# Performance work log

Hardware: AMD Instinct MI355X
Metric: run time of the kernel (lower is better)

The kernel has to match this reference:

```python
import jax, jax.numpy as jnp
import numpy as np

V, C, H, L, BLK = 32000, 1024, 16, 4, 1024
B, T = 4, 1024
FF = 100
HD = C // H
EPS = 1e-5


def setup_inputs() -> dict:
    key = jax.random.key(0)
    ks = jax.random.split(key, 16)
    n = lambda k, s: (jax.random.normal(k, s, dtype=jnp.float32) * 0.02)
    inp = {
        "idx": jax.random.randint(ks[0], (B, T), 0, V),
        "tok_emb": n(ks[1], (V, C)),
        "pos_emb": n(ks[2], (BLK, C)),
        "Wq": n(ks[3], (L, C, C)), "bq": jnp.zeros((L, C)),
        "Wk": n(ks[4], (L, C, C)), "bk": jnp.zeros((L, C)),
        "Wv": n(ks[5], (L, C, C)), "bv": jnp.zeros((L, C)),
        "Wo": n(ks[6], (L, C, C)), "bo": jnp.zeros((L, C)),
        "ln1_w": jnp.ones((L, C)), "ln1_b": jnp.zeros((L, C)),
        "ln2_w": jnp.ones((L, C)), "ln2_b": jnp.zeros((L, C)),
        "W1": n(ks[7], (L, C, FF)), "b1": jnp.zeros((L, FF)),
        "W2": n(ks[8], (L, FF, C)), "b2": jnp.zeros((L, C)),
        "lnf_w": jnp.ones((C,)), "lnf_b": jnp.zeros((C,)),
    }
    return inp


def _ln(x, w, b):
    m = jnp.mean(x, -1, keepdims=True)
    v = jnp.mean(jnp.square(x - m), -1, keepdims=True)
    return (x - m) * jax.lax.rsqrt(v + EPS) * w + b


def reference(idx, tok_emb, pos_emb, Wq, bq, Wk, bk, Wv, bv, Wo, bo,
              ln1_w, ln1_b, ln2_w, ln2_b, W1, b1, W2, b2, lnf_w, lnf_b):
    Bn, Tn = idx.shape
    x = tok_emb[idx] + pos_emb[:Tn][None]  # [B,T,C]; dropout is identity at eval
    scale = 1.0 / np.sqrt(HD).astype(np.float32)
    att_maps = []
    for l in range(L):
        h = _ln(x, ln1_w[l], ln1_b[l])
        q = (h @ Wq[l] + bq[l]).reshape(Bn, Tn, H, HD).transpose(0, 2, 1, 3)
        k = (h @ Wk[l] + bk[l]).reshape(Bn, Tn, H, HD).transpose(0, 2, 1, 3)
        v = (h @ Wv[l] + bv[l]).reshape(Bn, Tn, H, HD).transpose(0, 2, 1, 3)
        att = jax.nn.softmax(jnp.einsum("bhqd,bhkd->bhqk", q, k) * scale, axis=-1)
        y = jnp.einsum("bhqk,bhkd->bhqd", att, v).transpose(0, 2, 1, 3).reshape(Bn, Tn, C)
        x = x + (y @ Wo[l] + bo[l])
        f = _ln(x, ln2_w[l], ln2_b[l])
        f = jax.nn.relu(f @ W1[l] + b1[l]) @ W2[l] + b2[l]
        x = x + f
        att_maps.append(att.mean(0))  # [H,T,T]
    x = _ln(x, lnf_w, lnf_b)
    pooled = x.mean(1)  # [B,C]
    return pooled, jnp.stack(att_maps)  # [L,H,T,T]
```

## Files before the change

### kernel.cpp

```cpp
#include <hip/hip_runtime.h>

typedef __bf16 bf16;
typedef __bf16 bf16x4 __attribute__((ext_vector_type(4)));
typedef __bf16 bf16x8 __attribute__((ext_vector_type(8)));
typedef float  f32x4  __attribute__((ext_vector_type(4)));

static constexpr int kC   = 1024;
static constexpr int kT   = 1024;
static constexpr int kB   = 4;
static constexpr int kH   = 16;
static constexpr int kHD  = 64;
static constexpr int kL   = 4;
static constexpr int kFF  = 100;
static constexpr int kFFP = 128;
static constexpr int kM   = kB * kT;

__device__ __forceinline__ void gload16(const bf16* g, bf16* l)
{
    __builtin_amdgcn_global_load_lds(
        (const __attribute__((address_space(1))) void*)g,
        (__attribute__((address_space(3))) void*)l, 16, 0, 0);
}

__device__ __forceinline__ unsigned bpack(float a, float b)
{
    bf16 x = (bf16)a, y = (bf16)b;
    unsigned short ux = __builtin_bit_cast(unsigned short, x);
    unsigned short uy = __builtin_bit_cast(unsigned short, y);
    return (unsigned)ux | ((unsigned)uy << 16);
}
__device__ __forceinline__ float blo(unsigned u) { return __builtin_bit_cast(float, u << 16); }
__device__ __forceinline__ float bhi(unsigned u) { return __builtin_bit_cast(float, u & 0xffff0000u); }

__global__ __launch_bounds__(256)
void prep_kernel(const float* __restrict__ Wq, const float* __restrict__ Wk,
                 const float* __restrict__ Wv, const float* __restrict__ Wo,
                 const float* __restrict__ W1, const float* __restrict__ W2,
                 const float* __restrict__ bq, const float* __restrict__ bk,
                 const float* __restrict__ bv,
                 bf16* __restrict__ WQKVT, bf16* __restrict__ WOT,
                 bf16* __restrict__ W1T, bf16* __restrict__ W2T,
                 float* __restrict__ BQKV, float* __restrict__ pooled)
{
    __shared__ float tile[32][33];
    const int bid = blockIdx.x, tid = threadIdx.x;
    const float* src; bf16* dst; int K, N, KP, NP, bx, by;
    if (bid < 12288) {
        const int slab = bid >> 10, within = bid & 1023;
        const int l = slab / 3, which = slab % 3;
        const float* W = (which == 0) ? Wq : (which == 1) ? Wk : Wv;
        src = W + (long)l * kC * kC;
        dst = WQKVT + (long)l * 3 * kC * kC + (long)which * kC * kC;
        K = N = KP = NP = kC; bx = within & 31; by = within >> 5;
    } else if (bid < 16384) {
        const int t = bid - 12288, z = t >> 10, within = t & 1023;
        src = Wo + (long)z * kC * kC; dst = WOT + (long)z * kC * kC;
        K = N = KP = NP = kC; bx = within & 31; by = within >> 5;
    } else if (bid < 16896) {
        const int t = bid - 16384, z = t >> 7, within = t & 127;
        src = W1 + (long)z * kC * kFF; dst = W1T + (long)z * kFFP * kC;
        K = kC; N = kFF; KP = kC; NP = kFFP; bx = within & 3; by = within >> 2;
    } else if (bid < 17408) {
        const int t = bid - 16896, z = t >> 7, within = t & 127;
        src = W2 + (long)z * kFF * kC; dst = W2T + (long)z * kC * kFFP;
        K = kFF; N = kC; KP = kFFP; NP = kC; bx = within & 31; by = within >> 5;
    } else if (bid < 17456) {
        const int gid = (bid - 17408) * 256 + tid;
        const int l = gid / (3 * kC), wq = (gid / kC) % 3, c = gid & (kC - 1);
        const float* s = (wq == 0) ? bq : (wq == 1) ? bk : bv;
        BQKV[gid] = s[l * kC + c];
        return;
    } else {
        const int i = (bid - 17456) * 256 + tid;
        if (i < kB * kC) pooled[i] = 0.f;
        return;
    }
    const int n0 = bx * 32, k0 = by * 32;
    const int tx = tid & 31, ty = tid >> 5;
#pragma unroll
    for (int i = 0; i < 4; ++i) {
        int k = k0 + ty + i * 8, n = n0 + tx;
        tile[ty + i * 8][tx] = (k < K && n < N) ? src[(long)k * N + n] : 0.f;
    }
    __syncthreads();
#pragma unroll
    for (int i = 0; i < 4; ++i) {
        int n = n0 + ty + i * 8, k = k0 + tx;
        if (n < NP && k < KP) dst[(long)n * KP + k] = (bf16)tile[tx][ty + i * 8];
    }
}

__global__ __launch_bounds__(256)
void embed_kernel(const int* __restrict__ idx, const float* __restrict__ tok,
                  const float* __restrict__ pos, float* __restrict__ x)
{
    const int m = blockIdx.x;
    const int c = threadIdx.x * 4;
    const int t = m & (kT - 1);
    const long tk = (long)idx[m] * kC;
    float4 a = *(const float4*)&tok[tk + c];
    float4 b = *(const float4*)&pos[(long)t * kC + c];
    float4 o; o.x = a.x + b.x; o.y = a.y + b.y; o.z = a.z + b.z; o.w = a.w + b.w;
    *(float4*)&x[(long)m * kC + c] = o;
}

__global__ __launch_bounds__(256)
void ln_kernel(const float* __restrict__ x, const float* __restrict__ g,
               const float* __restrict__ be, bf16* __restrict__ ob)
{
    __shared__ float red[8];
    const long row = blockIdx.x;
    const int tid = threadIdx.x, lane = tid & 63, wv = tid >> 6;
    const float4 v = *(const float4*)&x[row * kC + tid * 4];
    float s = v.x + v.y + v.z + v.w;
    float s2 = v.x * v.x + v.y * v.y + v.z * v.z + v.w * v.w;
#pragma unroll
    for (int o = 32; o > 0; o >>= 1) { s += __shfl_down(s, o); s2 += __shfl_down(s2, o); }
    if (!lane) { red[wv] = s; red[4 + wv] = s2; }
    __syncthreads();
    s  = red[0] + red[1] + red[2] + red[3];
    s2 = red[4] + red[5] + red[6] + red[7];
    const float mean = s * (1.f / kC);
    const float var  = s2 * (1.f / kC) - mean * mean;
    const float rstd = rsqrtf(var + 1e-5f);
    const float4 gg = *(const float4*)&g[tid * 4];
    const float4 bb = *(const float4*)&be[tid * 4];
    bf16x4 o;
    o[0] = (bf16)((v.x - mean) * rstd * gg.x + bb.x);
    o[1] = (bf16)((v.y - mean) * rstd * gg.y + bb.y);
    o[2] = (bf16)((v.z - mean) * rstd * gg.z + bb.z);
    o[3] = (bf16)((v.w - mean) * rstd * gg.w + bb.w);
    *(bf16x4*)&ob[row * kC + tid * 4] = o;
}

template<int WAVES_M, int WAVES_N, int AI, int BJ, int MODE, int GL>
__global__ __launch_bounds__(256)
void gemm_bf16(const bf16* __restrict__ Ag, long strideA,
               const bf16* __restrict__ Bg, long strideB,
               const float* __restrict__ bias, int strideBias,
               bf16* __restrict__ outb, long strideOut,
               float* __restrict__ resid,
               int N, int K, int lda, int ldb)
{
    constexpr int BM = WAVES_M * AI * 16;
    constexpr int BN = WAVES_N * BJ * 16;
    constexpr int BK = 64;
    constexpr int LK = GL ? BK : (BK + 8);
    __shared__ __align__(16) bf16 As[BM * LK];
    __shared__ __align__(16) bf16 Bs[BN * LK];
    const int tid = threadIdx.x, lane = tid & 63, wv = tid >> 6;
    const int wm = wv / WAVES_N, wn = wv % WAVES_N;
    const int lr = lane & 15, lg = lane >> 4;
    const int z = blockIdx.z;
    const bf16* A = Ag + (long)z * strideA;
    const bf16* B = Bg + (long)z * strideB;
    const float* bi = bias ? bias + (long)z * strideBias : nullptr;
    const int m0 = blockIdx.y * BM, n0 = blockIdx.x * BN;

    f32x4 acc[AI][BJ];
#pragma unroll
    for (int i = 0; i < AI; ++i)
#pragma unroll
        for (int j = 0; j < BJ; ++j) acc[i][j] = (f32x4){0.f, 0.f, 0.f, 0.f};

    for (int k0 = 0; k0 < K; k0 += BK) {
        if constexpr (GL) {
            static_assert((BM % 32) == 0 && (BN % 32) == 0, "GL tile multiple of 32");
            const int sr  = lane >> 3;
            const int gcb = (lane & 7) ^ sr;
            constexpr int ARW = BM / 4;
            constexpr int BRW = BN / 4;
#pragma unroll
            for (int p = 0; p < BM / 32; ++p)
                gload16(A + (long)(m0 + wv * ARW + p * 8 + sr) * lda + k0 + gcb * 8,
                        &As[(wv * ARW + p * 8) * BK]);
#pragma unroll
            for (int p = 0; p < BN / 32; ++p)
                gload16(B + (long)(n0 + wv * BRW + p * 8 + sr) * ldb + k0 + gcb * 8,
                        &Bs[(wv * BRW + p * 8) * BK]);
        } else {
            constexpr int AP = (BM * BK) / (256 * 8);
#pragma unroll
            for (int p = 0; p < AP; ++p) {
                int r = p * 32 + (tid >> 3), c = (tid & 7) * 8;
                *(uint4*)&As[r * LK + c] = *(const uint4*)&A[(long)(m0 + r) * lda + k0 + c];
            }
            constexpr int BP = (BN * BK) / (256 * 8);
#pragma unroll
            for (int p = 0; p < BP; ++p) {
                int r = p * 32 + (tid >> 3), c = (tid & 7) * 8;
                *(uint4*)&Bs[r * LK + c] = *(const uint4*)&B[(long)(n0 + r) * ldb + k0 + c];
            }
        }
        __syncthreads();
#pragma unroll
        for (int kk = 0; kk < 2; ++kk) {
            bf16x8 af[AI], bfv[BJ];
#pragma unroll
            for (int i = 0; i < AI; ++i) {
                const int r = wm * AI * 16 + i * 16 + lr;
                const int c = GL ? (((kk * 4 + lg) ^ (lr & 7)) * 8) : (kk * 32 + lg * 8);
                af[i] = *(const bf16x8*)&As[r * LK + c];
            }
#pragma unroll
            for (int j = 0; j < BJ; ++j) {
                const int r = wn * BJ * 16 + j * 16 + lr;
                const int c = GL ? (((kk * 4 + lg) ^ (lr & 7)) * 8) : (kk * 32 + lg * 8);
                bfv[j] = *(const bf16x8*)&Bs[r * LK + c];
            }
#pragma unroll
            for (int i = 0; i < AI; ++i)
#pragma unroll
                for (int j = 0; j < BJ; ++j)
                    acc[i][j] = __builtin_amdgcn_mfma_f32_16x16x32_bf16(af[i], bfv[j], acc[i][j], 0, 0, 0);
        }
        __syncthreads();
    }

#pragma unroll
    for (int i = 0; i < AI; ++i)
#pragma unroll
        for (int j = 0; j < BJ; ++j)
#pragma unroll
            for (int rr = 0; rr < 4; ++rr) {
                const int grow = m0 + wm * AI * 16 + i * 16 + lg * 4 + rr;
                const int gcol = n0 + wn * BJ * 16 + j * 16 + lr;
                float v = acc[i][j][rr];
                if constexpr (MODE == 0) {
                    v += bi[gcol];
                    if (z == 0) v *= 0.125f * 1.44269504f;
                    const int b = grow >> 10, t = grow & (kT - 1);
                    const int hh = gcol >> 6, hd = gcol & 63;
                    long o = (long)z * strideOut;
                    if (z == 2) o += (((long)b * kH + hh) * kHD + hd) * kT + t;
                    else        o += (((long)b * kH + hh) * kT + t) * kHD + hd;
                    outb[o] = (bf16)v;
                } else {
                    v += bi[gcol];
                    resid[(long)grow * N + gcol] += v;
                }
            }
}

__global__ __launch_bounds__(256, 2)
void ff_fused(float* __restrict__ X, const float* __restrict__ g,
              const float* __restrict__ be,
              const bf16* __restrict__ W1T_, const float* __restrict__ b1_,
              const bf16* __restrict__ W2T_, const float* __restrict__ b2_)
{
    __shared__ __align__(16) bf16 Hs[16 * kC];
    __shared__ __align__(16) bf16 F1s[16 * kFFP];
    const int tid = threadIdx.x, lane = tid & 63, w = tid >> 6;
    const int lr = lane & 15, lg = lane >> 4;
    const int r0 = blockIdx.x * 16;

    {
        const int row = tid >> 4, c16 = tid & 15;
        float4 xv[16];
        float s1 = 0.f, s2 = 0.f;
#pragma unroll
        for (int p = 0; p < 8; ++p) {
            const float* base = &X[(long)(r0 + row) * kC + p * 128 + c16 * 8];
            xv[2 * p]     = *(const float4*)base;
            xv[2 * p + 1] = *(const float4*)(base + 4);
#pragma unroll
            for (int e = 0; e < 4; ++e) {
                float a0 = ((const float*)&xv[2 * p])[e], a1 = ((const float*)&xv[2 * p + 1])[e];
                s1 += a0 + a1; s2 += a0 * a0 + a1 * a1;
            }
        }
#pragma unroll
        for (int off = 1; off < 16; off <<= 1) { s1 += __shfl_xor(s1, off); s2 += __shfl_xor(s2, off); }
        const float mean = s1 * (1.f / kC);
        const float rstd = rsqrtf(s2 * (1.f / kC) - mean * mean + 1e-5f);
#pragma unroll
        for (int p = 0; p < 8; ++p) {
            const int c0 = p * 128 + c16 * 8;
            float4 g0 = *(const float4*)&g[c0],  g1 = *(const float4*)&g[c0 + 4];
            float4 b0 = *(const float4*)&be[c0], b1v = *(const float4*)&be[c0 + 4];
            float h[8];
#pragma unroll
            for (int e = 0; e < 4; ++e) {
                h[e]     = (((const float*)&xv[2 * p])[e]     - mean) * rstd * ((const float*)&g0)[e] + ((const float*)&b0)[e];
                h[4 + e] = (((const float*)&xv[2 * p + 1])[e] - mean) * rstd * ((const float*)&g1)[e] + ((const float*)&b1v)[e];
            }
            uint4 hv;
            hv.x = bpack(h[0], h[1]); hv.y = bpack(h[2], h[3]);
            hv.z = bpack(h[4], h[5]); hv.w = bpack(h[6], h[7]);
            const int cb = c16 + p * 16;
            *(uint4*)&Hs[row * kC + ((cb ^ (row & 7)) << 3)] = hv;
        }
    }
    __syncthreads();

    {
        f32x4 accA[2], accB[2];
#pragma unroll
        for (int j = 0; j < 2; ++j) { accA[j] = (f32x4){0,0,0,0}; accB[j] = (f32x4){0,0,0,0}; }
        for (int k0 = 0; k0 < kC; k0 += 64) {
            const bf16x8 a0 = *(const bf16x8*)&Hs[lr * kC + ((((k0 >> 3) + 0 * 4 + lg) ^ (lr & 7)) << 3)];
            const bf16x8 a1 = *(const bf16x8*)&Hs[lr * kC + ((((k0 >> 3) + 1 * 4 + lg) ^ (lr & 7)) << 3)];
#pragma unroll
            for (int j = 0; j < 2; ++j) {
                const bf16x8 b0 = *(const bf16x8*)&W1T_[(long)(w * 32 + j * 16 + lr) * kC + k0 + 0 * 32 + lg * 8];
                const bf16x8 b1 = *(const bf16x8*)&W1T_[(long)(w * 32 + j * 16 + lr) * kC + k0 + 1 * 32 + lg * 8];
                accA[j] = __builtin_amdgcn_mfma_f32_16x16x32_bf16(a0, b0, accA[j], 0, 0, 0);
                accB[j] = __builtin_amdgcn_mfma_f32_16x16x32_bf16(a1, b1, accB[j], 0, 0, 0);
            }
        }
#pragma unroll
        for (int j = 0; j < 2; ++j)
#pragma unroll
            for (int rr = 0; rr < 4; ++rr) {
                const int row = lg * 4 + rr, col = w * 32 + j * 16 + lr;
                float v = accA[j][rr] + accB[j][rr] + (col < kFF ? b1_[col] : 0.f);
                F1s[row * kFFP + (((col >> 3) ^ (row & 7)) << 3) + (col & 7)] = (bf16)fmaxf(v, 0.f);
            }
    }
    __syncthreads();

    for (int nc = 0; nc < 8; ++nc) {
        f32x4 acc[2];
        acc[0] = (f32x4){0.f, 0.f, 0.f, 0.f};
        acc[1] = (f32x4){0.f, 0.f, 0.f, 0.f};
#pragma unroll
        for (int kk = 0; kk < 4; ++kk) {
            const bf16x8 a = *(const bf16x8*)&F1s[lr * kFFP + (((kk * 4 + lg) ^ (lr & 7)) << 3)];
#pragma unroll
            for (int j = 0; j < 2; ++j) {
                const bf16x8 bv = *(const bf16x8*)&W2T_[(long)(nc * 128 + w * 32 + j * 16 + lr) * kFFP + kk * 32 + lg * 8];
                acc[j] = __builtin_amdgcn_mfma_f32_16x16x32_bf16(a, bv, acc[j], 0, 0, 0);
            }
        }
#pragma unroll
        for (int j = 0; j < 2; ++j)
#pragma unroll
            for (int rr = 0; rr < 4; ++rr) {
                const int row = r0 + lg * 4 + rr, col = nc * 128 + w * 32 + j * 16 + lr;
                X[(long)row * kC + col] += acc[j][rr] + b2_[col];
            }
    }
}

__global__ __launch_bounds__(256, 2)
void attn_fused(const bf16* __restrict__ Qg, const bf16* __restrict__ Kg,
                const bf16* __restrict__ VTg, bf16* __restrict__ yg,
                float* __restrict__ attm)
{
    __shared__ __align__(16) bf16 SH[32768];
    bf16* Klds = SH;
    bf16* Vlds = SH + 8192;
    bf16* Ps   = SH + 16384;
    __shared__ __align__(16) float reds[16][4];
    __shared__ float invs[16];
    const int tid = threadIdx.x, lane = tid & 63, w = tid >> 6;
    const int lr = lane & 15, lg = lane >> 4;
    const int bid = blockIdx.x, r_ = bid >> 3;
    const int h = ((bid & 7) << 1) | (r_ & 1);
    const int q0 = (r_ >> 1) * 16;

    const int sr  = lane >> 3;
    const int gcb = (lane & 7) ^ sr;
    const int loB = (lg & 1) * 4;

    unsigned am_[16][2];
#pragma unroll
    for (int j = 0; j < 16; ++j) { am_[j][0] = 0u; am_[j][1] = 0u; }

    for (int b = 0; b < kB; ++b) {
        const long bh = (long)b * kH + h;
        const bf16* Qb = Qg + (bh * kT + q0) * kHD;
        const bf16* Kb = Kg + bh * kT * kHD;
        const bf16* Vb = VTg + bh * (long)kHD * kT;

        const bf16x8 qf0 = *(const bf16x8*)&Qb[lr * kHD + lg * 8];
        const bf16x8 qf1 = *(const bf16x8*)&Qb[lr * kHD + 32 + lg * 8];

        {
            const int rowb = w * 16 + sr;
            gload16(Kb + (rowb)     * kHD + gcb * 8, &Klds[(w * 16) * 64]);
            gload16(Kb + (rowb + 8) * kHD + gcb * 8, &Klds[(w * 16 + 8) * 64]);
            gload16(Vb + (long)(rowb)     * kT + gcb * 8, &Vlds[(w * 16) * 64]);
            gload16(Vb + (long)(rowb + 8) * kT + gcb * 8, &Vlds[(w * 16 + 8) * 64]);
        }
        __syncthreads();

        float s = 0.f;
        f32x4 y0 = (f32x4){0.f, 0.f, 0.f, 0.f};
        f32x4 y1 = (f32x4){0.f, 0.f, 0.f, 0.f};

        for (int kt = 0; kt < 16; ++kt) {
            const int cur = (kt & 1) * 4096;
            if (kt < 15) {
                const int nxt = 4096 - cur;
                const int kn = (kt + 1) * 64;
                const int rowb = w * 16 + sr;
                gload16(Kb + (kn + rowb)     * kHD + gcb * 8, &Klds[nxt + (w * 16) * 64]);
                gload16(Kb + (kn + rowb + 8) * kHD + gcb * 8, &Klds[nxt + (w * 16 + 8) * 64]);
                gload16(Vb + (long)(rowb)     * kT + kn + gcb * 8, &Vlds[nxt + (w * 16) * 64]);
                gload16(Vb + (long)(rowb + 8) * kT + kn + gcb * 8, &Vlds[nxt + (w * 16 + 8) * 64]);
            }
            const int krow = w * 16 + lr;
            const bf16x8 kf0 = *(const bf16x8*)&Klds[cur + krow * 64 + (((0 + lg) ^ (lr & 7)) << 3)];
            const bf16x8 kf1 = *(const bf16x8*)&Klds[cur + krow * 64 + (((4 + lg) ^ (lr & 7)) << 3)];
            f32x4 a = (f32x4){0.f, 0.f, 0.f, 0.f};
            a = __builtin_amdgcn_mfma_f32_16x16x32_bf16(kf0, qf0, a, 0, 0, 0);
            a = __builtin_amdgcn_mfma_f32_16x16x32_bf16(kf1, qf1, a, 0, 0, 0);
            const float e0 = exp2f(a[0]), e1 = exp2f(a[1]);
            const float e2 = exp2f(a[2]), e3 = exp2f(a[3]);
            s += (e0 + e1) + (e2 + e3);
            const int tb = kt * 8 + w * 2 + (lg >> 1);
            uint2 pk; pk.x = bpack(e0, e1); pk.y = bpack(e2, e3);
            *(uint2*)&Ps[lr * kT + ((tb ^ (lr & 7)) << 3) + loB] = pk;
            __syncthreads();
            const int vrow = w * 16 + lr;
            const bf16x8 a0 = *(const bf16x8*)&Ps[lr * kT + (((kt * 8 + 0 + lg) ^ (lr & 7)) << 3)];
            const bf16x8 v0 = *(const bf16x8*)&Vlds[cur + vrow * 64 + (((0 + lg) ^ (lr & 7)) << 3)];
            const bf16x8 a1 = *(const bf16x8*)&Ps[lr * kT + (((kt * 8 + 4 + lg) ^ (lr & 7)) << 3)];
            const bf16x8 v1 = *(const bf16x8*)&Vlds[cur + vrow * 64 + (((4 + lg) ^ (lr & 7)) << 3)];
            y0 = __builtin_amdgcn_mfma_f32_16x16x32_bf16(a0, v0, y0, 0, 0, 0);
            y1 = __builtin_amdgcn_mfma_f32_16x16x32_bf16(a1, v1, y1, 0, 0, 0);
            __syncthreads();
        }

        s += __shfl_xor(s, 16);
        s += __shfl_xor(s, 32);
        if (lane < 16) reds[lane][w] = s;
        __syncthreads();
        float4 rv = *(const float4*)&reds[lr][0];
        const float inv = __builtin_amdgcn_rcpf((rv.x + rv.y) + (rv.z + rv.w));
        const float iv4 = inv * 0.25f;
        if (lane < 16) invs[lane] = inv;

#pragma unroll
        for (int kt = 0; kt < 16; ++kt) {
            const int tb = kt * 8 + w * 2 + (lg >> 1);
            uint2 e2v = *(const uint2*)&Ps[lr * kT + ((tb ^ (lr & 7)) << 3) + loB];
#pragma unroll
            for (int d = 0; d < 2; ++d) {
                unsigned ev = d ? e2v.y : e2v.x;
                unsigned av = am_[kt][d];
                float n0 = blo(av) + blo(ev) * iv4;
                float n1 = bhi(av) + bhi(ev) * iv4;
                am_[kt][d] = bpack(n0, n1);
            }
        }

#pragma unroll
        for (int rr = 0; rr < 4; ++rr) {
            const float iv = invs[lg * 4 + rr];
            yg[((long)b * kT + q0 + lg * 4 + rr) * kC + h * kHD + w * 16 + lr]
                = (bf16)((y0[rr] + y1[rr]) * iv);
        }
    }

    __syncthreads();
    float* amf = (float*)SH;
#pragma unroll
    for (int kt = 0; kt < 16; ++kt)
#pragma unroll
        for (int d = 0; d < 2; ++d) {
            unsigned av = am_[kt][d];
            const int col = kt * 64 + w * 16 + lg * 4 + 2 * d;
            amf[lr * kT + col]     = blo(av);
            amf[lr * kT + col + 1] = bhi(av);
        }
    __syncthreads();
#pragma unroll
    for (int p = 0; p < 16; ++p) {
        const int f = p * 256 + tid;
        const int row = f >> 8, c4 = f & 255;
        float4 v = *(const float4*)&amf[row * kT + c4 * 4];
        *(float4*)&attm[((long)h * kT + q0 + row) * kT + c4 * 4] = v;
    }
}

__global__ __launch_bounds__(256)
void pool_kernel(const bf16* __restrict__ hb, float* __restrict__ pooled)
{
    const int c = blockIdx.x * 256 + threadIdx.x;
    const int b = blockIdx.y;
    const int t0 = blockIdx.z * 128;
    float s = 0.f;
    for (int t = t0; t < t0 + 128; ++t) s += (float)hb[((long)b * kT + t) * kC + c];
    atomicAdd(&pooled[b * kC + c], s * (1.f / kT));
}

extern "C" void kernel_launch(void* const* d_in, const int* in_sizes, int n_in,
                              void* d_out, int out_size, void* d_ws, size_t ws_size,
                              hipStream_t stream)
{
    const int*   idx  = (const int*)d_in[0];
    const float* tok  = (const float*)d_in[1];
    const float* pos  = (const float*)d_in[2];
    const float* Wq   = (const float*)d_in[3];
    const float* bq   = (const float*)d_in[4];
    const float* Wk   = (const float*)d_in[5];
    const float* bk   = (const float*)d_in[6];
    const float* Wv   = (const float*)d_in[7];
    const float* bv   = (const float*)d_in[8];
    const float* Wo   = (const float*)d_in[9];
    const float* bo   = (const float*)d_in[10];
    const float* ln1w = (const float*)d_in[11];
    const float* ln1b = (const float*)d_in[12];
    const float* ln2w = (const float*)d_in[13];
    const float* ln2b = (const float*)d_in[14];
    const float* W1   = (const float*)d_in[15];
    const float* b1   = (const float*)d_in[16];
    const float* W2   = (const float*)d_in[17];
    const float* b2   = (const float*)d_in[18];
    const float* lnfw = (const float*)d_in[19];
    const float* lnfb = (const float*)d_in[20];

    char* ws = (char*)d_ws;
    long off = 0;
    auto alloc = [&](long bytes) { char* p = ws + off; off += (bytes + 255) & ~255L; return p; };
    bf16*  WQKVT = (bf16*)alloc((long)kL * 3 * kC * kC * 2);
    bf16*  WOT   = (bf16*)alloc((long)kL * kC * kC * 2);
    bf16*  W1T   = (bf16*)alloc((long)kL * kFFP * kC * 2);
    bf16*  W2T   = (bf16*)alloc((long)kL * kC * kFFP * 2);
    float* BQKV  = (float*)alloc((long)kL * 3 * kC * 4);
    float* X     = (float*)alloc((long)kM * kC * 4);
    bf16*  Hbuf  = (bf16*)alloc((long)kM * kC * 2);
    bf16*  QKV   = (bf16*)alloc(3L * kM * kC * 2);
    bf16*  Y     = (bf16*)alloc((long)kM * kC * 2);

    float* pooled = (float*)d_out;
    float* attm_base = pooled + kB * kC;

    prep_kernel<<<17472, 256, 0, stream>>>(Wq, Wk, Wv, Wo, W1, W2, bq, bk, bv,
                                           WQKVT, WOT, W1T, W2T, BQKV, pooled);
    embed_kernel<<<kM, 256, 0, stream>>>(idx, tok, pos, X);

    for (int l = 0; l < kL; ++l) {
        ln_kernel<<<kM, 256, 0, stream>>>(X, ln1w + l * kC, ln1b + l * kC, Hbuf);
        gemm_bf16<2, 2, 4, 4, 0, 1><<<dim3(8, 32, 3), 256, 0, stream>>>(
            Hbuf, 0L, WQKVT + (long)l * 3 * kC * kC, (long)kC * kC,
            BQKV + l * 3 * kC, kC, QKV, (long)kM * kC, nullptr,
            kC, kC, kC, kC);
        attn_fused<<<dim3(1024), 256, 0, stream>>>(
            QKV, QKV + (long)kM * kC, QKV + 2L * kM * kC, Y,
            attm_base + (long)l * kH * kT * kT);
        gemm_bf16<2, 2, 4, 4, 4, 1><<<dim3(8, 32, 1), 256, 0, stream>>>(
            Y, 0L, WOT + (long)l * kC * kC, 0L, bo + l * kC, 0,
            nullptr, 0L, X, kC, kC, kC, kC);
        ff_fused<<<256, 256, 0, stream>>>(X, ln2w + l * kC, ln2b + l * kC,
                                          W1T + (long)l * kFFP * kC, b1 + l * kFF,
                                          W2T + (long)l * kC * kFFP, b2 + l * kC);
    }
    ln_kernel<<<kM, 256, 0, stream>>>(X, lnfw, lnfb, Hbuf);
    pool_kernel<<<dim3(4, kB, 8), 256, 0, stream>>>(Hbuf, pooled);
}
```

Before: 916.1 us.

## Prefetch next batch K/V tile and drop per-iteration trailing barrier in attention

The attention kernel now issues the first K/V tile load for the next batch during the last key tile of the current batch, so the double buffer runs continuously across the batch loop instead of stalling at each batch start. The trailing __syncthreads in each key-tile iteration is removed. This relies on each wave reading only the K/V rows it loaded itself, guarded by explicit s_waitcnt vmcnt counts. The mid-iteration barrier becomes an lgkmcnt wait plus a raw s_barrier with sched_barrier fences, and the key loop is fully unrolled. The risks are fragile hand-counted vmcnt waits and higher register pressure from the unroll.

```diff
diff --git a/kernel.cpp b/kernel.cpp
--- a/kernel.cpp
+++ b/kernel.cpp
@@ -362,44 +362,60 @@
     const int sr  = lane >> 3;
     const int gcb = (lane & 7) ^ sr;
     const int loB = (lg & 1) * 4;
+    const int rowb = w * 16 + sr;
+    const int ldK0 = (w * 16) * 64, ldK1 = (w * 16 + 8) * 64;
 
     unsigned am_[16][2];
 #pragma unroll
     for (int j = 0; j < 16; ++j) { am_[j][0] = 0u; am_[j][1] = 0u; }
+
+    {
+        const bf16* Kb0 = Kg + (long)h * kT * kHD;
+        const bf16* Vb0 = VTg + (long)h * kHD * kT;
+        gload16(Kb0 + (rowb)     * kHD + gcb * 8, &Klds[ldK0]);
+        gload16(Kb0 + (rowb + 8) * kHD + gcb * 8, &Klds[ldK1]);
+        gload16(Vb0 + (long)(rowb)     * kT + gcb * 8, &Vlds[ldK0]);
+        gload16(Vb0 + (long)(rowb + 8) * kT + gcb * 8, &Vlds[ldK1]);
+    }
 
     for (int b = 0; b < kB; ++b) {
         const long bh = (long)b * kH + h;
         const bf16* Qb = Qg + (bh * kT + q0) * kHD;
         const bf16* Kb = Kg + bh * kT * kHD;
         const bf16* Vb = VTg + bh * (long)kHD * kT;
+        const bf16* Kbn = Kg + (bh + kH) * kT * kHD;
+        const bf16* Vbn = VTg + (bh + kH) * (long)kHD * kT;
 
         const bf16x8 qf0 = *(const bf16x8*)&Qb[lr * kHD + lg * 8];
         const bf16x8 qf1 = *(const bf16x8*)&Qb[lr * kHD + 32 + lg * 8];
-
-        {
-            const int rowb = w * 16 + sr;
-            gload16(Kb + (rowb)     * kHD + gcb * 8, &Klds[(w * 16) * 64]);
-            gload16(Kb + (rowb + 8) * kHD + gcb * 8, &Klds[(w * 16 + 8) * 64]);
-            gload16(Vb + (long)(rowb)     * kT + gcb * 8, &Vlds[(w * 16) * 64]);
-            gload16(Vb + (long)(rowb + 8) * kT + gcb * 8, &Vlds[(w * 16 + 8) * 64]);
-        }
-        __syncthreads();
 
         float s = 0.f;
         f32x4 y0 = (f32x4){0.f, 0.f, 0.f, 0.f};
         f32x4 y1 = (f32x4){0.f, 0.f, 0.f, 0.f};
 
+#pragma unroll
         for (int kt = 0; kt < 16; ++kt) {
-            const int cur = (kt & 1) * 4096;
+            const int cur = ((b * 16 + kt) & 1) * 4096;
+            const int nxt = 4096 - cur;
             if (kt < 15) {
-                const int nxt = 4096 - cur;
                 const int kn = (kt + 1) * 64;
-                const int rowb = w * 16 + sr;
-                gload16(Kb + (kn + rowb)     * kHD + gcb * 8, &Klds[nxt + (w * 16) * 64]);
-                gload16(Kb + (kn + rowb + 8) * kHD + gcb * 8, &Klds[nxt + (w * 16 + 8) * 64]);
-                gload16(Vb + (long)(rowb)     * kT + kn + gcb * 8, &Vlds[nxt + (w * 16) * 64]);
-                gload16(Vb + (long)(rowb + 8) * kT + kn + gcb * 8, &Vlds[nxt + (w * 16 + 8) * 64]);
-            }
+                gload16(Kb + (kn + rowb)     * kHD + gcb * 8, &Klds[nxt + ldK0]);
+                gload16(Kb + (kn + rowb + 8) * kHD + gcb * 8, &Klds[nxt + ldK1]);
+                gload16(Vb + (long)(rowb)     * kT + kn + gcb * 8, &Vlds[nxt + ldK0]);
+                gload16(Vb + (long)(rowb + 8) * kT + kn + gcb * 8, &Vlds[nxt + ldK1]);
+            } else if (b < kB - 1) {
+                gload16(Kbn + (rowb)     * kHD + gcb * 8, &Klds[nxt + ldK0]);
+                gload16(Kbn + (rowb + 8) * kHD + gcb * 8, &Klds[nxt + ldK1]);
+                gload16(Vbn + (long)(rowb)     * kT + gcb * 8, &Vlds[nxt + ldK0]);
+                gload16(Vbn + (long)(rowb + 8) * kT + gcb * 8, &Vlds[nxt + ldK1]);
+            }
+            if (kt == 15 && b == kB - 1) {
+                asm volatile("s_waitcnt vmcnt(0)" ::: "memory");
+            } else {
+                asm volatile("s_waitcnt vmcnt(4)" ::: "memory");
+            }
+            __builtin_amdgcn_sched_barrier(0);
+
             const int krow = w * 16 + lr;
             const bf16x8 kf0 = *(const bf16x8*)&Klds[cur + krow * 64 + (((0 + lg) ^ (lr & 7)) << 3)];
             const bf16x8 kf1 = *(const bf16x8*)&Klds[cur + krow * 64 + (((4 + lg) ^ (lr & 7)) << 3)];
@@ -412,7 +428,11 @@
             const int tb = kt * 8 + w * 2 + (lg >> 1);
             uint2 pk; pk.x = bpack(e0, e1); pk.y = bpack(e2, e3);
             *(uint2*)&Ps[lr * kT + ((tb ^ (lr & 7)) << 3) + loB] = pk;
-            __syncthreads();
+
+            asm volatile("s_waitcnt lgkmcnt(0)" ::: "memory");
+            __builtin_amdgcn_s_barrier();
+            __builtin_amdgcn_sched_barrier(0);
+
             const int vrow = w * 16 + lr;
             const bf16x8 a0 = *(const bf16x8*)&Ps[lr * kT + (((kt * 8 + 0 + lg) ^ (lr & 7)) << 3)];
             const bf16x8 v0 = *(const bf16x8*)&Vlds[cur + vrow * 64 + (((0 + lg) ^ (lr & 7)) << 3)];
@@ -420,13 +440,14 @@
             const bf16x8 v1 = *(const bf16x8*)&Vlds[cur + vrow * 64 + (((4 + lg) ^ (lr & 7)) << 3)];
             y0 = __builtin_amdgcn_mfma_f32_16x16x32_bf16(a0, v0, y0, 0, 0, 0);
             y1 = __builtin_amdgcn_mfma_f32_16x16x32_bf16(a1, v1, y1, 0, 0, 0);
-            __syncthreads();
         }
 
         s += __shfl_xor(s, 16);
         s += __shfl_xor(s, 32);
         if (lane < 16) reds[lane][w] = s;
-        __syncthreads();
+        asm volatile("s_waitcnt lgkmcnt(0)" ::: "memory");
+        __builtin_amdgcn_s_barrier();
+        __builtin_amdgcn_sched_barrier(0);
         float4 rv = *(const float4*)&reds[lr][0];
         const float inv = __builtin_amdgcn_rcpf((rv.x + rv.y) + (rv.z + rv.w));
         const float iv4 = inv * 0.25f;
```

Result: no change. 900.2 us (-1.7%).

## Stage K/V tiles through registers with 128-key tiles and fewer barriers

Applied to the files above, without the earlier changes.

The attention kernel now processes 128 keys per iteration instead of 64, which halves the number of loop trips and block barriers. It replaces asynchronous global-to-LDS loads and double-buffered LDS with register prefetch of the next K/V tile, written into a single LDS buffer after the PV MFMAs. Per-iteration syncs become a raw s_barrier plus lgkmcnt wait, so one barrier per tile is removed. This adds register pressure from the prefetch registers. With a single buffer, correctness depends on every wave having finished its reads before the overwrite, and only one barrier per iteration guards that.

```diff
diff --git a/kernel.cpp b/kernel.cpp
--- a/kernel.cpp
+++ b/kernel.cpp
@@ -362,6 +362,7 @@
     const int sr  = lane >> 3;
     const int gcb = (lane & 7) ^ sr;
     const int loB = (lg & 1) * 4;
+    const int wr8 = lane * 8;
 
     unsigned am_[16][2];
 #pragma unroll
@@ -376,75 +377,108 @@
         const bf16x8 qf0 = *(const bf16x8*)&Qb[lr * kHD + lg * 8];
         const bf16x8 qf1 = *(const bf16x8*)&Qb[lr * kHD + 32 + lg * 8];
 
-        {
-            const int rowb = w * 16 + sr;
-            gload16(Kb + (rowb)     * kHD + gcb * 8, &Klds[(w * 16) * 64]);
-            gload16(Kb + (rowb + 8) * kHD + gcb * 8, &Klds[(w * 16 + 8) * 64]);
-            gload16(Vb + (long)(rowb)     * kT + gcb * 8, &Vlds[(w * 16) * 64]);
-            gload16(Vb + (long)(rowb + 8) * kT + gcb * 8, &Vlds[(w * 16 + 8) * 64]);
-        }
-        __syncthreads();
+        uint4 kR[4], vR[4];
+#pragma unroll
+        for (int c = 0; c < 4; ++c) {
+            kR[c] = *(const uint4*)(Kb + (w * 32 + c * 8 + sr) * kHD + gcb * 8);
+            const int vr = w * 16 + c * 4 + (lane >> 4);
+            const int vs = (lane & 15) ^ ((c * 4 + (lane >> 4)) & 7);
+            vR[c] = *(const uint4*)(Vb + (long)vr * kT + vs * 8);
+        }
+#pragma unroll
+        for (int c = 0; c < 4; ++c) {
+            *(uint4*)&Klds[(w * 32 + c * 8) * 64 + wr8] = kR[c];
+            const int vr = w * 16 + c * 4 + (lane >> 4);
+            *(uint4*)&Vlds[vr * 128 + (lane & 15) * 8] = vR[c];
+        }
 
         float s = 0.f;
         f32x4 y0 = (f32x4){0.f, 0.f, 0.f, 0.f};
         f32x4 y1 = (f32x4){0.f, 0.f, 0.f, 0.f};
 
-        for (int kt = 0; kt < 16; ++kt) {
-            const int cur = (kt & 1) * 4096;
-            if (kt < 15) {
-                const int nxt = 4096 - cur;
-                const int kn = (kt + 1) * 64;
-                const int rowb = w * 16 + sr;
-                gload16(Kb + (kn + rowb)     * kHD + gcb * 8, &Klds[nxt + (w * 16) * 64]);
-                gload16(Kb + (kn + rowb + 8) * kHD + gcb * 8, &Klds[nxt + (w * 16 + 8) * 64]);
-                gload16(Vb + (long)(rowb)     * kT + kn + gcb * 8, &Vlds[nxt + (w * 16) * 64]);
-                gload16(Vb + (long)(rowb + 8) * kT + kn + gcb * 8, &Vlds[nxt + (w * 16 + 8) * 64]);
-            }
-            const int krow = w * 16 + lr;
-            const bf16x8 kf0 = *(const bf16x8*)&Klds[cur + krow * 64 + (((0 + lg) ^ (lr & 7)) << 3)];
-            const bf16x8 kf1 = *(const bf16x8*)&Klds[cur + krow * 64 + (((4 + lg) ^ (lr & 7)) << 3)];
-            f32x4 a = (f32x4){0.f, 0.f, 0.f, 0.f};
-            a = __builtin_amdgcn_mfma_f32_16x16x32_bf16(kf0, qf0, a, 0, 0, 0);
-            a = __builtin_amdgcn_mfma_f32_16x16x32_bf16(kf1, qf1, a, 0, 0, 0);
-            const float e0 = exp2f(a[0]), e1 = exp2f(a[1]);
-            const float e2 = exp2f(a[2]), e3 = exp2f(a[3]);
-            s += (e0 + e1) + (e2 + e3);
-            const int tb = kt * 8 + w * 2 + (lg >> 1);
-            uint2 pk; pk.x = bpack(e0, e1); pk.y = bpack(e2, e3);
-            *(uint2*)&Ps[lr * kT + ((tb ^ (lr & 7)) << 3) + loB] = pk;
-            __syncthreads();
+#pragma unroll
+        for (int kt = 0; kt < 8; ++kt) {
+            if (kt < 7) {
+                const int kn = (kt + 1) * 128;
+#pragma unroll
+                for (int c = 0; c < 4; ++c) {
+                    kR[c] = *(const uint4*)(Kb + (kn + w * 32 + c * 8 + sr) * kHD + gcb * 8);
+                    const int vr = w * 16 + c * 4 + (lane >> 4);
+                    const int vs = (lane & 15) ^ ((c * 4 + (lane >> 4)) & 7);
+                    vR[c] = *(const uint4*)(Vb + (long)vr * kT + kn + vs * 8);
+                }
+            }
+
+            f32x4 acc[2];
+            acc[0] = (f32x4){0.f, 0.f, 0.f, 0.f};
+            acc[1] = (f32x4){0.f, 0.f, 0.f, 0.f};
+#pragma unroll
+            for (int j2 = 0; j2 < 2; ++j2) {
+                const int krow = w * 32 + j2 * 16 + lr;
+                const bf16x8 kf0 = *(const bf16x8*)&Klds[krow * 64 + (((0 + lg) ^ (lr & 7)) << 3)];
+                const bf16x8 kf1 = *(const bf16x8*)&Klds[krow * 64 + (((4 + lg) ^ (lr & 7)) << 3)];
+                acc[j2] = __builtin_amdgcn_mfma_f32_16x16x32_bf16(kf0, qf0, acc[j2], 0, 0, 0);
+                acc[j2] = __builtin_amdgcn_mfma_f32_16x16x32_bf16(kf1, qf1, acc[j2], 0, 0, 0);
+            }
+#pragma unroll
+            for (int j2 = 0; j2 < 2; ++j2) {
+                const float e0 = exp2f(acc[j2][0]), e1 = exp2f(acc[j2][1]);
+                const float e2 = exp2f(acc[j2][2]), e3 = exp2f(acc[j2][3]);
+                s += (e0 + e1) + (e2 + e3);
+                const int tb = kt * 16 + w * 4 + j2 * 2 + (lg >> 1);
+                uint2 pk; pk.x = bpack(e0, e1); pk.y = bpack(e2, e3);
+                *(uint2*)&Ps[lr * kT + ((tb ^ (lr & 7)) << 3) + loB] = pk;
+            }
+
+            asm volatile("s_waitcnt lgkmcnt(0)" ::: "memory");
+            __builtin_amdgcn_s_barrier();
+            __builtin_amdgcn_sched_barrier(0);
+
             const int vrow = w * 16 + lr;
-            const bf16x8 a0 = *(const bf16x8*)&Ps[lr * kT + (((kt * 8 + 0 + lg) ^ (lr & 7)) << 3)];
-            const bf16x8 v0 = *(const bf16x8*)&Vlds[cur + vrow * 64 + (((0 + lg) ^ (lr & 7)) << 3)];
-            const bf16x8 a1 = *(const bf16x8*)&Ps[lr * kT + (((kt * 8 + 4 + lg) ^ (lr & 7)) << 3)];
-            const bf16x8 v1 = *(const bf16x8*)&Vlds[cur + vrow * 64 + (((4 + lg) ^ (lr & 7)) << 3)];
-            y0 = __builtin_amdgcn_mfma_f32_16x16x32_bf16(a0, v0, y0, 0, 0, 0);
-            y1 = __builtin_amdgcn_mfma_f32_16x16x32_bf16(a1, v1, y1, 0, 0, 0);
-            __syncthreads();
+#pragma unroll
+            for (int kc = 0; kc < 4; ++kc) {
+                const bf16x8 a = *(const bf16x8*)&Ps[lr * kT + (((kt * 16 + kc * 4 + lg) ^ (lr & 7)) << 3)];
+                const bf16x8 v = *(const bf16x8*)&Vlds[vrow * 128 + (((kc * 4 + lg) ^ (lr & 7)) << 3)];
+                if (kc & 1) y1 = __builtin_amdgcn_mfma_f32_16x16x32_bf16(a, v, y1, 0, 0, 0);
+                else        y0 = __builtin_amdgcn_mfma_f32_16x16x32_bf16(a, v, y0, 0, 0, 0);
+            }
+
+            if (kt < 7) {
+#pragma unroll
+                for (int c = 0; c < 4; ++c) {
+                    *(uint4*)&Klds[(w * 32 + c * 8) * 64 + wr8] = kR[c];
+                    const int vr = w * 16 + c * 4 + (lane >> 4);
+                    *(uint4*)&Vlds[vr * 128 + (lane & 15) * 8] = vR[c];
+                }
+            }
         }
 
         s += __shfl_xor(s, 16);
         s += __shfl_xor(s, 32);
         if (lane < 16) reds[lane][w] = s;
-        __syncthreads();
+        asm volatile("s_waitcnt lgkmcnt(0)" ::: "memory");
+        __builtin_amdgcn_s_barrier();
+        __builtin_amdgcn_sched_barrier(0);
         float4 rv = *(const float4*)&reds[lr][0];
         const float inv = __builtin_amdgcn_rcpf((rv.x + rv.y) + (rv.z + rv.w));
         const float iv4 = inv * 0.25f;
         if (lane < 16) invs[lane] = inv;
 
 #pragma unroll
-        for (int kt = 0; kt < 16; ++kt) {
-            const int tb = kt * 8 + w * 2 + (lg >> 1);
-            uint2 e2v = *(const uint2*)&Ps[lr * kT + ((tb ^ (lr & 7)) << 3) + loB];
-#pragma unroll
-            for (int d = 0; d < 2; ++d) {
-                unsigned ev = d ? e2v.y : e2v.x;
-                unsigned av = am_[kt][d];
-                float n0 = blo(av) + blo(ev) * iv4;
-                float n1 = bhi(av) + bhi(ev) * iv4;
-                am_[kt][d] = bpack(n0, n1);
-            }
-        }
+        for (int kt = 0; kt < 8; ++kt)
+#pragma unroll
+            for (int j2 = 0; j2 < 2; ++j2) {
+                const int tb = kt * 16 + w * 4 + j2 * 2 + (lg >> 1);
+                uint2 e2v = *(const uint2*)&Ps[lr * kT + ((tb ^ (lr & 7)) << 3) + loB];
+#pragma unroll
+                for (int d = 0; d < 2; ++d) {
+                    unsigned ev = d ? e2v.y : e2v.x;
+                    unsigned av = am_[kt * 2 + j2][d];
+                    float n0 = blo(av) + blo(ev) * iv4;
+                    float n1 = bhi(av) + bhi(ev) * iv4;
+                    am_[kt * 2 + j2][d] = bpack(n0, n1);
+                }
+            }
 
 #pragma unroll
         for (int rr = 0; rr < 4; ++rr) {
@@ -457,14 +491,16 @@
     __syncthreads();
     float* amf = (float*)SH;
 #pragma unroll
-    for (int kt = 0; kt < 16; ++kt)
-#pragma unroll
-        for (int d = 0; d < 2; ++d) {
-            unsigned av = am_[kt][d];
-            const int col = kt * 64 + w * 16 + lg * 4 + 2 * d;
-            amf[lr * kT + col]     = blo(av);
-            amf[lr * kT + col + 1] = bhi(av);
-        }
+    for (int kt = 0; kt < 8; ++kt)
+#pragma unroll
+        for (int j2 = 0; j2 < 2; ++j2)
+#pragma unroll
+            for (int d = 0; d < 2; ++d) {
+                unsigned av = am_[kt * 2 + j2][d];
+                const int col = kt * 128 + w * 32 + j2 * 16 + lg * 4 + 2 * d;
+                amf[lr * kT + col]     = blo(av);
+                amf[lr * kT + col + 1] = bhi(av);
+            }
     __syncthreads();
 #pragma unroll
     for (int p = 0; p < 16; ++p) {
```

Result: slower. 1.103 ms (+20.5%).
